# Kernel optimization log

Hardware: AMD Instinct MI355X
Metric: run time of the kernel (lower is better)

## Reference

```python
import jax, jax.numpy as jnp
import numpy as np

N = 100000   # nodes
E = 1600000  # edges
IN, HID, OUT = 128, 128, 64  # hidden = 2 * out_channels per GCNEncoder


def setup_inputs() -> dict:
    key = jax.random.key(0)
    k = jax.random.split(key, 5)
    x = jax.random.normal(k[0], (N, IN), dtype=jnp.float32)
    edge_index = jax.random.randint(k[1], (2, E), 0, N, dtype=jnp.int32)
    # Glorot-style init like PyG GCNConv
    W1 = jax.random.normal(k[2], (IN, HID), dtype=jnp.float32) * (1.0 / np.sqrt(IN))
    b1 = jnp.zeros((HID,), dtype=jnp.float32)
    W2 = jax.random.normal(k[3], (HID, OUT), dtype=jnp.float32) * (1.0 / np.sqrt(HID))
    b2 = jnp.zeros((OUT,), dtype=jnp.float32)
    return {"x": x, "edge_index": edge_index, "W1": W1, "b1": b1, "W2": W2, "b2": b2}


def gcn_conv(x, row, col, W, b):
    # x: [N, F_in]; row/col: [E+N] (edge_index with self-loops appended)
    h = x @ W                                      # dense transform [N, F_out]
    deg = jax.ops.segment_sum(jnp.ones_like(col, dtype=h.dtype), col, num_segments=N)
    dinv = jnp.where(deg > 0, jax.lax.rsqrt(deg), 0.0)
    norm = dinv[row] * dinv[col]                   # symmetric normalization per edge
    msg = h[row] * norm[:, None]                   # gather + scale: [E+N, F_out]
    out = jax.ops.segment_sum(msg, col, num_segments=N)  # scatter-add to targets
    return out + b


def reference(x, edge_index, W1, b1, W2, b2):
    loops = jnp.arange(N, dtype=edge_index.dtype)
    row = jnp.concatenate([edge_index[0], loops])  # sources
    col = jnp.concatenate([edge_index[1], loops])  # targets
    h = jax.nn.relu(gcn_conv(x, row, col, W1, b1))
    return gcn_conv(h, row, col, W2, b2)
```

## Files before the change

### kernel.cpp

```cpp
#include <hip/hip_runtime.h>
#include <hip/hip_fp16.h>

#define N_NODES 100000
#define N_EDGES 1600000
#define K_DIM   128

#define CHUNK_LG 8
#define CHUNK    256
#define NBKT     ((N_NODES + CHUNK - 1) / CHUNK)
#define CAP      4608
#define EPB      4096
#define NBLK_A   ((N_EDGES + EPB - 1) / EPB)
#define G1_BLOCKS ((N_NODES + 63) / 64)

typedef _Float16 half8 __attribute__((ext_vector_type(8)));
typedef float    f32x4 __attribute__((ext_vector_type(4)));

__global__ __launch_bounds__(256) void k_gemm1_bucket(
    const float* __restrict__ x, const float* __restrict__ W,
    _Float16* __restrict__ Hout,
    const int* __restrict__ row, const int* __restrict__ col,
    int* __restrict__ gcur, int* __restrict__ pairs)
{
    __shared__ __align__(16) char smem[128 * 136 * 2];

    if (blockIdx.x < G1_BLOCKS) {
        constexpr int KD = K_DIM, NOUT = 128, NT = NOUT / 16;
        _Float16 (*Blds)[KD + 8] = reinterpret_cast<_Float16(*)[KD + 8]>(smem);

        for (int i = threadIdx.x * 4; i < KD * NOUT; i += 256 * 4) {
            int k = i / NOUT, n = i % NOUT;
            float4 wv = *reinterpret_cast<const float4*>(W + i);
            Blds[n + 0][k] = (_Float16)wv.x;
            Blds[n + 1][k] = (_Float16)wv.y;
            Blds[n + 2][k] = (_Float16)wv.z;
            Blds[n + 3][k] = (_Float16)wv.w;
        }
        __syncthreads();

        const int wave = threadIdx.x >> 6;
        const int lane = threadIdx.x & 63;
        const int r16  = lane & 15;
        const int kg   = lane >> 4;
        const int arow = blockIdx.x * 64 + wave * 16 + r16;
        const bool rowok = arow < N_NODES;

        f32x4 acc[NT];
#pragma unroll
        for (int ct = 0; ct < NT; ++ct) acc[ct] = (f32x4){0.f, 0.f, 0.f, 0.f};

#pragma unroll
        for (int kc = 0; kc < KD / 32; ++kc) {
            const int k0 = kc * 32 + kg * 8;
            float4 xa = make_float4(0.f, 0.f, 0.f, 0.f), xb = xa;
            if (rowok) {
                const float4* ap = reinterpret_cast<const float4*>(
                    x + (size_t)arow * KD + k0);
                xa = ap[0]; xb = ap[1];
            }
            half8 a;
            a[0] = (_Float16)xa.x; a[1] = (_Float16)xa.y;
            a[2] = (_Float16)xa.z; a[3] = (_Float16)xa.w;
            a[4] = (_Float16)xb.x; a[5] = (_Float16)xb.y;
            a[6] = (_Float16)xb.z; a[7] = (_Float16)xb.w;
#pragma unroll
            for (int ct = 0; ct < NT; ++ct) {
                half8 b = *reinterpret_cast<const half8*>(&Blds[ct * 16 + r16][k0]);
                acc[ct] = __builtin_amdgcn_mfma_f32_16x16x32_f16(a, b, acc[ct], 0, 0, 0);
            }
        }

        const int orow0 = blockIdx.x * 64 + wave * 16 + kg * 4;
#pragma unroll
        for (int r = 0; r < 4; ++r) {
            int orow = orow0 + r;
            if (orow < N_NODES) {
#pragma unroll
                for (int ct = 0; ct < NT; ++ct)
                    Hout[(size_t)orow * NOUT + ct * 16 + r16] = (_Float16)acc[ct][r];
            }
        }
    } else {
        int* hist  = (int*)smem;
        int* sbase = hist + 512;
        int* lcur  = hist + 1024;
        int t = threadIdx.x;
        for (int i = t; i < NBKT; i += 256) { hist[i] = 0; lcur[i] = 0; }
        __syncthreads();
        int base = (blockIdx.x - G1_BLOCKS) * EPB;
        int myb[16], myp[16];
#pragma unroll
        for (int j = 0; j < 16; ++j) {
            int i = base + t + j * 256;
            int b = -1, p = 0;
            if (i < N_EDGES) {
                int r = row[i], c = col[i];
                b = c >> CHUNK_LG;
                p = ((c & (CHUNK - 1)) << 17) | r;
                atomicAdd(&hist[b], 1);
            }
            myb[j] = b; myp[j] = p;
        }
        __syncthreads();
        for (int i = t; i < NBKT; i += 256) {
            int c = hist[i];
            sbase[i] = c ? atomicAdd(&gcur[i], c) : 0;
        }
        __syncthreads();
#pragma unroll
        for (int j = 0; j < 16; ++j) {
            int b = myb[j];
            if (b >= 0) {
                int pos = sbase[b] + atomicAdd(&lcur[b], 1);
                pairs[b * CAP + pos] = myp[j];
            }
        }
    }
}

__global__ __launch_bounds__(256) void k_fillB(const int* __restrict__ gcur,
                                               const int* __restrict__ pairs,
                                               int* __restrict__ rowptr,
                                               float* __restrict__ dinv,
                                               int* __restrict__ srows) {
    __shared__ int red[256];
    __shared__ int psum[256];
    __shared__ int deg[CHUNK];
    __shared__ int curs[CHUNK];
    int b = blockIdx.x, t = threadIdx.x;

    int part = 0;
    for (int i = t; i < NBKT; i += 256)
        if (i < b) part += gcur[i];
    red[t] = part;
    __syncthreads();
    for (int off = 128; off; off >>= 1) {
        if (t < off) red[t] += red[t + off];
        __syncthreads();
    }
    int gb = red[0];
    int cnt = gcur[b];
    if (b == 0 && t == 0) rowptr[N_NODES] = N_EDGES;

    int nbase = b << CHUNK_LG;
    const int* mp = pairs + b * CAP;

    deg[t] = 0;
    __syncthreads();
    for (int i = t; i < cnt; i += 256) atomicAdd(&deg[mp[i] >> 17], 1);
    __syncthreads();

    int d = deg[t];
    psum[t] = d;
    __syncthreads();
    for (int off = 1; off < 256; off <<= 1) {
        int u = (t >= off) ? psum[t - off] : 0;
        __syncthreads();
        psum[t] += u;
        __syncthreads();
    }
    int o = gb + psum[t] - d;
    curs[t] = o;
    int node = nbase + t;
    if (node < N_NODES) {
        rowptr[node] = o;
        dinv[node] = rsqrtf(1.f + (float)d);
    }
    __syncthreads();
    for (int i = t; i < cnt; i += 256) {
        int v = mp[i];
        int pos = atomicAdd(&curs[v >> 17], 1);
        srows[pos] = v & 0x1FFFF;
    }
}

template<int NOUT>
__global__ __launch_bounds__(256) void k_gemm_mfma2(
    const _Float16* __restrict__ Ah, const float* __restrict__ W,
    const float* __restrict__ b_in, _Float16* __restrict__ Hout, int nrows)
{
    constexpr int KD = K_DIM;
    constexpr int NT = NOUT / 16;
    __shared__ _Float16 Blds[NOUT][KD + 8];

    for (int i = threadIdx.x * 4; i < KD * NOUT; i += 256 * 4) {
        int k = i / NOUT, n = i % NOUT;
        float4 wv = *reinterpret_cast<const float4*>(W + i);
        Blds[n + 0][k] = (_Float16)wv.x;
        Blds[n + 1][k] = (_Float16)wv.y;
        Blds[n + 2][k] = (_Float16)wv.z;
        Blds[n + 3][k] = (_Float16)wv.w;
    }
    __syncthreads();

    const int wave = threadIdx.x >> 6;
    const int lane = threadIdx.x & 63;
    const int r16  = lane & 15;
    const int kg   = lane >> 4;
    const int arow = blockIdx.x * 64 + wave * 16 + r16;
    const bool rowok = arow < nrows;

    f32x4 acc[NT];
#pragma unroll
    for (int ct = 0; ct < NT; ++ct) acc[ct] = (f32x4){0.f, 0.f, 0.f, 0.f};

#pragma unroll
    for (int kc = 0; kc < KD / 32; ++kc) {
        const int k0 = kc * 32 + kg * 8;
        uint4 raw = make_uint4(0, 0, 0, 0);
        if (rowok)
            raw = *reinterpret_cast<const uint4*>(Ah + (size_t)arow * KD + k0);
        union { uint4 u; _Float16 h[8]; } U; U.u = raw;
        float4 bA = *reinterpret_cast<const float4*>(b_in + k0);
        float4 bB = *reinterpret_cast<const float4*>(b_in + k0 + 4);
        half8 a;
        a[0] = (_Float16)fmaxf((float)U.h[0] + bA.x, 0.f);
        a[1] = (_Float16)fmaxf((float)U.h[1] + bA.y, 0.f);
        a[2] = (_Float16)fmaxf((float)U.h[2] + bA.z, 0.f);
        a[3] = (_Float16)fmaxf((float)U.h[3] + bA.w, 0.f);
        a[4] = (_Float16)fmaxf((float)U.h[4] + bB.x, 0.f);
        a[5] = (_Float16)fmaxf((float)U.h[5] + bB.y, 0.f);
        a[6] = (_Float16)fmaxf((float)U.h[6] + bB.z, 0.f);
        a[7] = (_Float16)fmaxf((float)U.h[7] + bB.w, 0.f);
#pragma unroll
        for (int ct = 0; ct < NT; ++ct) {
            half8 b = *reinterpret_cast<const half8*>(&Blds[ct * 16 + r16][k0]);
            acc[ct] = __builtin_amdgcn_mfma_f32_16x16x32_f16(a, b, acc[ct], 0, 0, 0);
        }
    }

    const int orow0 = blockIdx.x * 64 + wave * 16 + kg * 4;
#pragma unroll
    for (int r = 0; r < 4; ++r) {
        int orow = orow0 + r;
        if (orow < nrows) {
#pragma unroll
            for (int ct = 0; ct < NT; ++ct)
                Hout[(size_t)orow * NOUT + ct * 16 + r16] = (_Float16)acc[ct][r];
        }
    }
}

__device__ __forceinline__ void fma8(uint4 v, float wgt, float (&acc)[8]) {
    union { uint4 u; _Float16 h[8]; } U;
    U.u = v;
#pragma unroll
    for (int j = 0; j < 8; ++j)
        acc[j] = fmaf((float)U.h[j], wgt, acc[j]);
}

template<int F, bool OUT_HALF>
__global__ __launch_bounds__(256) void k_gather_h(
    const int* __restrict__ rowptr, const int* __restrict__ srows,
    const float* __restrict__ dinv, const _Float16* __restrict__ H,
    const float* __restrict__ bias, void* __restrict__ OUT, int n)
{
    constexpr int LPR = F / 8;
    constexpr int GR  = 64 / LPR;
    int w = blockIdx.x * 4 + (threadIdx.x >> 6);
    if (w >= n) return;
    int lane = threadIdx.x & 63;
    int g = lane / LPR;
    int c = lane % LPR;
    float di = dinv[w];
    int s = rowptr[w], e = rowptr[w + 1];
    const uint4* Hp = reinterpret_cast<const uint4*>(H);

    float acc[8];
#pragma unroll
    for (int j = 0; j < 8; ++j) acc[j] = 0.f;
    uint4 hv = Hp[(size_t)w * LPR + c];
    fma8(hv, (g == 0) ? di * di : 0.f, acc);

    for (int k = s; k < e; k += 2 * GR) {
        int k0 = k + g, k1 = k + GR + g;
        int kk0 = min(k0, e - 1), kk1 = min(k1, e - 1);
        int r0 = srows[kk0], r1 = srows[kk1];
        float w0 = (k0 < e) ? dinv[r0] * di : 0.f;
        float w1 = (k1 < e) ? dinv[r1] * di : 0.f;
        uint4 h0 = Hp[(size_t)r0 * LPR + c];
        uint4 h1 = Hp[(size_t)r1 * LPR + c];
        fma8(h0, w0, acc);
        fma8(h1, w1, acc);
    }

#pragma unroll
    for (int m = 32; m >= LPR; m >>= 1) {
#pragma unroll
        for (int j = 0; j < 8; ++j)
            acc[j] += __shfl_xor(acc[j], m, 64);
    }

    if (g == 0) {
        if constexpr (OUT_HALF) {
            union { uint4 u; __half2 h[4]; } P;
#pragma unroll
            for (int j = 0; j < 4; ++j)
                P.h[j] = __floats2half2_rn(acc[2 * j], acc[2 * j + 1]);
            reinterpret_cast<uint4*>(OUT)[(size_t)w * LPR + c] = P.u;
        } else {
            const float4* bp = reinterpret_cast<const float4*>(bias + c * 8);
            float4 b0 = bp[0], b1 = bp[1];
            float4 o0 = make_float4(acc[0] + b0.x, acc[1] + b0.y,
                                    acc[2] + b0.z, acc[3] + b0.w);
            float4 o1 = make_float4(acc[4] + b1.x, acc[5] + b1.y,
                                    acc[6] + b1.z, acc[7] + b1.w);
            float* op = (float*)OUT + (size_t)w * F + c * 8;
            *reinterpret_cast<float4*>(op)     = o0;
            *reinterpret_cast<float4*>(op + 4) = o1;
        }
    }
}


extern "C" void kernel_launch(void* const* d_in, const int* in_sizes, int n_in,
                              void* d_out, int out_size, void* d_ws, size_t ws_size,
                              hipStream_t stream) {
    const float* x  = (const float*)d_in[0];
    const int*   ei = (const int*)  d_in[1];
    const float* W1 = (const float*)d_in[2];
    const float* b1 = (const float*)d_in[3];
    const float* W2 = (const float*)d_in[4];
    const float* b2 = (const float*)d_in[5];
    float* out = (float*)d_out;

    const int* row = ei;
    const int* col = ei + N_EDGES;

    char* ws = (char*)d_ws;
    int*   gcur   = (int*)ws;
    int*   rowptr = gcur + 512;
    float* dinv   = (float*)(rowptr + ((N_NODES + 256) & ~255));
    int*   srows  = (int*)(dinv + ((N_NODES + 255) & ~255));
    _Float16* bufH   = (_Float16*)(srows + ((N_EDGES + 255) & ~255));
    _Float16* bufAgg = bufH + (size_t)N_NODES * 128;
    int*   pairs  = (int*)bufAgg;

    hipMemsetAsync(gcur, 0, NBKT * sizeof(int), stream);
    k_gemm1_bucket<<<G1_BLOCKS + NBLK_A, 256, 0, stream>>>(
        x, W1, bufH, row, col, gcur, pairs);

    k_fillB<<<NBKT, 256, 0, stream>>>(gcur, pairs, rowptr, dinv, srows);

    k_gather_h<128, true><<<(N_NODES + 3) / 4, 256, 0, stream>>>(
        rowptr, srows, dinv, bufH, nullptr, bufAgg, N_NODES);

    k_gemm_mfma2<64><<<(N_NODES + 63) / 64, 256, 0, stream>>>(
        bufAgg, W2, b1, bufH, N_NODES);

    k_gather_h<64, false><<<(N_NODES + 3) / 4, 256, 0, stream>>>(
        rowptr, srows, dinv, bufH, b2, out, N_NODES);
}
```

Measured before the change: 201.1 us.

## Interleave GEMM and bucketing blocks, shrink edges per block, software-pipeline gather

```diff
diff --git a/kernel.cpp b/kernel.cpp
--- a/kernel.cpp
+++ b/kernel.cpp
@@ -9,7 +9,7 @@
 #define CHUNK    256
 #define NBKT     ((N_NODES + CHUNK - 1) / CHUNK)
 #define CAP      4608
-#define EPB      4096
+#define EPB      1024
 #define NBLK_A   ((N_EDGES + EPB - 1) / EPB)
 #define G1_BLOCKS ((N_NODES + 63) / 64)
 
@@ -24,7 +24,7 @@
 {
     __shared__ __align__(16) char smem[128 * 136 * 2];
 
-    if (blockIdx.x < G1_BLOCKS) {
+    if (blockIdx.x & 1) {
         constexpr int KD = K_DIM, NOUT = 128, NT = NOUT / 16;
         _Float16 (*Blds)[KD + 8] = reinterpret_cast<_Float16(*)[KD + 8]>(smem);
 
@@ -38,11 +38,12 @@
         }
         __syncthreads();
 
+        const int tile = blockIdx.x >> 1;
         const int wave = threadIdx.x >> 6;
         const int lane = threadIdx.x & 63;
         const int r16  = lane & 15;
         const int kg   = lane >> 4;
-        const int arow = blockIdx.x * 64 + wave * 16 + r16;
+        const int arow = tile * 64 + wave * 16 + r16;
         const bool rowok = arow < N_NODES;
 
         f32x4 acc[NT];
@@ -70,7 +71,7 @@
             }
         }
 
-        const int orow0 = blockIdx.x * 64 + wave * 16 + kg * 4;
+        const int orow0 = tile * 64 + wave * 16 + kg * 4;
 #pragma unroll
         for (int r = 0; r < 4; ++r) {
             int orow = orow0 + r;
@@ -87,10 +88,10 @@
         int t = threadIdx.x;
         for (int i = t; i < NBKT; i += 256) { hist[i] = 0; lcur[i] = 0; }
         __syncthreads();
-        int base = (blockIdx.x - G1_BLOCKS) * EPB;
-        int myb[16], myp[16];
-#pragma unroll
-        for (int j = 0; j < 16; ++j) {
+        int base = (blockIdx.x >> 1) * EPB;
+        int myb[4], myp[4];
+#pragma unroll
+        for (int j = 0; j < 4; ++j) {
             int i = base + t + j * 256;
             int b = -1, p = 0;
             if (i < N_EDGES) {
@@ -108,7 +109,7 @@
         }
         __syncthreads();
 #pragma unroll
-        for (int j = 0; j < 16; ++j) {
+        for (int j = 0; j < 4; ++j) {
             int b = myb[j];
             if (b >= 0) {
                 int pos = sbase[b] + atomicAdd(&lcur[b], 1);
@@ -272,16 +273,22 @@
     uint4 hv = Hp[(size_t)w * LPR + c];
     fma8(hv, (g == 0) ? di * di : 0.f, acc);
 
-    for (int k = s; k < e; k += 2 * GR) {
-        int k0 = k + g, k1 = k + GR + g;
-        int kk0 = min(k0, e - 1), kk1 = min(k1, e - 1);
-        int r0 = srows[kk0], r1 = srows[kk1];
-        float w0 = (k0 < e) ? dinv[r0] * di : 0.f;
-        float w1 = (k1 < e) ? dinv[r1] * di : 0.f;
-        uint4 h0 = Hp[(size_t)r0 * LPR + c];
-        uint4 h1 = Hp[(size_t)r1 * LPR + c];
-        fma8(h0, w0, acc);
-        fma8(h1, w1, acc);
+    if (s < e) {
+        int k0 = s + g;
+        int kc = min(k0, e - 1);
+        int r  = srows[kc];
+        float wcur = (k0 < e) ? dinv[r] * di : 0.f;
+        uint4 hcur = Hp[(size_t)r * LPR + c];
+        for (int k = s + GR; k < e; k += GR) {
+            int k1  = k + g;
+            int kc1 = min(k1, e - 1);
+            int r1  = srows[kc1];
+            float wnxt = (k1 < e) ? dinv[r1] * di : 0.f;
+            uint4 hnxt = Hp[(size_t)r1 * LPR + c];
+            fma8(hcur, wcur, acc);
+            wcur = wnxt; hcur = hnxt;
+        }
+        fma8(hcur, wcur, acc);
     }
 
 #pragma unroll
```

Result: slower. 216.5 us (+7.6%).
